# Performance work log

Hardware: AMD Instinct MI355X
Metric: run time of the kernel (lower is better)

## Reference

```python
import jax, jax.numpy as jnp
import numpy as np

B, T = 32, 64
INPUT_DIM, EMB, HA, HB, NUM_CLASS = 4894, 128, 128, 128, 1
D_IN = EMB + 1  # use_time=True appends scalar time feature


def gru_cell(x, h, Wih, Whh, bih, bhh):
    # torch nn.GRU cell semantics, gate order (r, z, n)
    gi = x @ Wih.T + bih
    gh = h @ Whh.T + bhh
    ir, iz, i_n = jnp.split(gi, 3, axis=-1)
    hr, hz, hn = jnp.split(gh, 3, axis=-1)
    r = jax.nn.sigmoid(ir + hr)
    z = jax.nn.sigmoid(iz + hz)
    n = jnp.tanh(i_n + r * hn)
    return (1.0 - z) * n + z * h


def setup_inputs():
    key = jax.random.key(0)
    ks = jax.random.split(key, 14)
    f32 = jnp.float32
    s = lambda k, sh, sc: (jax.random.normal(k, sh) * sc).astype(f32)
    return {
        "x": jax.random.uniform(ks[0], (B, T, INPUT_DIM), dtype=f32),
        "t": jax.random.uniform(ks[1], (B, T), dtype=f32),
        "lengths": jax.random.randint(ks[2], (B,), 1, T + 1),
        "W_emb": s(ks[3], (EMB, INPUT_DIM), 0.02),
        "Wih_a": s(ks[4], (3 * HA, D_IN), 0.05),
        "Whh_a": s(ks[5], (3 * HA, HA), 0.05),
        "bih_a": jnp.zeros((3 * HA,), f32),
        "bhh_a": jnp.zeros((3 * HA,), f32),
        "Wih_b": s(ks[6], (3 * HB, D_IN), 0.05),
        "Whh_b": s(ks[7], (3 * HB, HB), 0.05),
        "bih_b": jnp.zeros((3 * HB,), f32),
        "bhh_b": jnp.zeros((3 * HB,), f32),
        "w_alpha": s(ks[8], (1, HA), 0.1),
        "b_alpha": jnp.zeros((1,), f32),
        "W_beta": s(ks[9], (EMB, HB), 0.1),
        "b_beta": jnp.zeros((EMB,), f32),
        "W_out": s(ks[10], (NUM_CLASS, EMB), 0.1),
        "b_out": jnp.zeros((NUM_CLASS,), f32),
    }


def reference(x, t, lengths, W_emb, Wih_a, Whh_a, bih_a, bhh_a,
              Wih_b, Whh_b, bih_b, bhh_b, w_alpha, b_alpha,
              W_beta, b_beta, W_out, b_out):
    # embedding (dropout is identity in inference)
    emb = x @ W_emb.T                                   # [B,T,E]
    temb = jnp.concatenate([emb, t[..., None]], axis=-1)  # [B,T,E+1]

    # reversed-prefix tensor: R[b,i,k] = temb[b, i-k] for k<=i else 0
    i_idx = jnp.arange(T)[:, None]
    k_idx = jnp.arange(T)[None, :]
    src = i_idx - k_idx                                  # [T,T]
    valid = (src >= 0)
    src_c = jnp.clip(src, 0)
    vmask = valid[None, :, :, None].astype(emb.dtype)
    R = jnp.take(temb, src_c, axis=1) * vmask            # [B,T,T,D_IN]
    E_rev = jnp.take(emb, src_c, axis=1) * vmask         # [B,T,T,E]

    # run alpha/beta GRUs along the prefix axis k (causal, so zero padding
    # at k>i never affects the k<=i outputs that we keep)
    R_k = jnp.moveaxis(R, 2, 0)                          # [Tk,B,T,D_IN]
    h0a = jnp.zeros((B, T, HA), emb.dtype)
    h0b = jnp.zeros((B, T, HB), emb.dtype)

    def step(carry, xk):
        ha, hb = carry
        ha = gru_cell(xk, ha, Wih_a, Whh_a, bih_a, bhh_a)
        hb = gru_cell(xk, hb, Wih_b, Whh_b, bih_b, bhh_b)
        return (ha, hb), (ha, hb)

    _, (Ha, Hb) = jax.lax.scan(step, (h0a, h0b), R_k)
    Ha = jnp.moveaxis(Ha, 0, 2)                          # [B,T,Tk,HA]
    Hb = jnp.moveaxis(Hb, 0, 2)                          # [B,T,Tk,HB]

    # attention over the i+1 prefix positions
    scores = (Ha @ w_alpha.T + b_alpha)[..., 0]          # [B,T,Tk]
    scores = jnp.where(valid[None], scores, jnp.float32(-1e9))
    alpha = jax.nn.softmax(scores, axis=-1)
    beta = jnp.tanh(Hb @ W_beta.T + b_beta)              # [B,T,Tk,E]

    c = jnp.einsum('btk,btke,btke->bte', alpha, beta, E_rev)
    row_valid = (jnp.arange(T)[None, :] < lengths[:, None]).astype(c.dtype)
    c = c * row_valid[..., None]                         # zero where i >= lengths[b]

    logits = c @ W_out.T + b_out                         # [B,T,1]
    return logits[..., 0]
```

## Files before the change

### kernel.cpp

```cpp
#include <hip/hip_runtime.h>
#include <hip/hip_bf16.h>

#define DEVI __device__ __forceinline__

typedef __attribute__((ext_vector_type(8))) short short8;
typedef __attribute__((ext_vector_type(8))) unsigned short ushort8;
typedef __attribute__((ext_vector_type(4))) unsigned short ushort4v;
typedef __attribute__((ext_vector_type(2))) unsigned int u32x2;
typedef __attribute__((ext_vector_type(4))) float f32x4;

static constexpr int TT = 64, KIN = 4894, KINP = 4896, E = 128;
static constexpr float L2E = 1.4426950408889634f;

DEVI unsigned short f2bf(float f) {
    union { float f; unsigned u; } v; v.f = f;
    unsigned r = v.u + 0x7fffu + ((v.u >> 16) & 1u);
    return (unsigned short)(r >> 16);
}
DEVI float sigm2(float x) { return __builtin_amdgcn_rcpf(1.f + __builtin_amdgcn_exp2f(-x)); }
DEVI float tanh2(float x) { return 1.f - 2.f * __builtin_amdgcn_rcpf(__builtin_amdgcn_exp2f(x + x) + 1.f); }

DEVI void bar_lds() {
    asm volatile("s_waitcnt lgkmcnt(0)" ::: "memory");
    __builtin_amdgcn_s_barrier();
}

DEVI short8 cvt8(const float* __restrict__ p, float s) {
    float2 v0 = *(const float2*)p, v1 = *(const float2*)(p + 2);
    float2 v2 = *(const float2*)(p + 4), v3 = *(const float2*)(p + 6);
    short8 r;
    r[0] = (short)f2bf(v0.x * s); r[1] = (short)f2bf(v0.y * s);
    r[2] = (short)f2bf(v1.x * s); r[3] = (short)f2bf(v1.y * s);
    r[4] = (short)f2bf(v2.x * s); r[5] = (short)f2bf(v2.y * s);
    r[6] = (short)f2bf(v3.x * s); r[7] = (short)f2bf(v3.y * s);
    return r;
}

__global__ void prep_kernel(const float* __restrict__ Wemb,
                            const float* __restrict__ Wih_a, const float* __restrict__ Wih_b,
                            const float* __restrict__ Whh_a, const float* __restrict__ Whh_b,
                            const float* __restrict__ Wbeta,
                            unsigned short* __restrict__ wembbf, unsigned short* __restrict__ wihbf,
                            unsigned short* __restrict__ whhbf, unsigned short* __restrict__ wbetabf) {
    int job = blockIdx.x * blockDim.x + threadIdx.x;
    const int JWE = 128 * 612, JWIH = 768 * 16, JWHH = 768 * 16, JWB = 128 * 16;
    if (job < JWE) {
        int row = job / 612, c8 = (job % 612) * 8;
        ushort8 v;
        #pragma unroll
        for (int jj = 0; jj < 8; ++jj) { int c = c8 + jj; v[jj] = (c < KIN) ? f2bf(Wemb[(long)row * KIN + c]) : (unsigned short)0; }
        *(ushort8*)(wembbf + (long)row * KINP + c8) = v;
        return;
    }
    job -= JWE;
    if (job < JWIH) {
        int g = job / 16, c8 = (job % 16) * 8;
        const float* src = (g < 384) ? (Wih_a + (long)g * 129) : (Wih_b + (long)(g - 384) * 129);
        ushort8 v;
        #pragma unroll
        for (int jj = 0; jj < 8; ++jj) v[jj] = f2bf(src[c8 + jj] * L2E);
        *(ushort8*)(wihbf + (long)g * 128 + c8) = v;
        return;
    }
    job -= JWIH;
    if (job < JWHH) {
        int g = job / 16, c8 = (job % 16) * 8;
        const float* src = (g < 384) ? (Whh_a + (long)g * 128) : (Whh_b + (long)(g - 384) * 128);
        ushort8 v;
        #pragma unroll
        for (int jj = 0; jj < 8; ++jj) v[jj] = f2bf(src[c8 + jj] * L2E);
        *(ushort8*)(whhbf + (long)g * 128 + c8) = v;
        return;
    }
    job -= JWHH;
    if (job < JWB) {
        int e = job / 16, c8 = (job % 16) * 8;
        ushort8 v;
        #pragma unroll
        for (int jj = 0; jj < 8; ++jj) v[jj] = f2bf(Wbeta[(long)e * 128 + c8 + jj] * L2E);
        *(ushort8*)(wbetabf + (long)e * 128 + c8) = v;
    }
}

__global__ __launch_bounds__(256) void emb_gemm(const float* __restrict__ x,
                                                const unsigned short* __restrict__ wembbf,
                                                float* __restrict__ pout) {
    const int ks = blockIdx.x & 3, m0 = (blockIdx.x >> 2) * 16;
    const int w = threadIdx.x >> 6, l = threadIdx.x & 63, lr = l & 15, lo = l >> 4;
    const int n0 = (2 * w) * 16 + lr, n1 = (2 * w + 1) * 16 + lr;
    const float* xrow = x + (long)(m0 + lr) * KIN;
    const int k0 = ks * 1216;
    f32x4 acc0 = {0, 0, 0, 0}, acc1 = {0, 0, 0, 0};
    #pragma unroll 2
    for (int kt = 0; kt < 38; ++kt) {
        int k = k0 + kt * 32 + lo * 8;
        short8 a = cvt8(xrow + k, 1.f);
        short8 b0 = *(const short8*)(wembbf + (long)n0 * KINP + k);
        short8 b1 = *(const short8*)(wembbf + (long)n1 * KINP + k);
        acc0 = __builtin_amdgcn_mfma_f32_16x16x32_bf16(a, b0, acc0, 0, 0, 0);
        acc1 = __builtin_amdgcn_mfma_f32_16x16x32_bf16(a, b1, acc1, 0, 0, 0);
    }
    if (ks == 3) {
        int k = 4864 + lo * 8;
        short8 a;
        #pragma unroll
        for (int jj = 0; jj < 8; ++jj) { int c = k + jj; a[jj] = (c < KIN) ? (short)f2bf(xrow[c]) : (short)0; }
        short8 b0 = *(const short8*)(wembbf + (long)n0 * KINP + k);
        short8 b1 = *(const short8*)(wembbf + (long)n1 * KINP + k);
        acc0 = __builtin_amdgcn_mfma_f32_16x16x32_bf16(a, b0, acc0, 0, 0, 0);
        acc1 = __builtin_amdgcn_mfma_f32_16x16x32_bf16(a, b1, acc1, 0, 0, 0);
    }
    float* pbase = pout + (long)ks * 2048 * E;
    #pragma unroll
    for (int r = 0; r < 4; ++r) {
        int m = m0 + lo * 4 + r;
        pbase[(long)m * E + n0] = acc0[r];
        pbase[(long)m * E + n1] = acc1[r];
    }
}

__global__ __launch_bounds__(256) void emb_reduce(const float* __restrict__ pout,
                                                  float* __restrict__ emb, unsigned short* __restrict__ embbf) {
    const long idx = (long)blockIdx.x * 256 + threadIdx.x;
    const long base = idx * 4;
    f32x4 s = *(const f32x4*)(pout + base);
    #pragma unroll
    for (int ks = 1; ks < 4; ++ks) {
        f32x4 v = *(const f32x4*)(pout + (long)ks * 2048 * E + base);
        s[0] += v[0]; s[1] += v[1]; s[2] += v[2]; s[3] += v[3];
    }
    *(f32x4*)(emb + base) = s;
    ushort4v h;
    #pragma unroll
    for (int jj = 0; jj < 4; ++jj) h[jj] = f2bf(s[jj]);
    *(ushort4v*)(embbf + base) = h;
}

__global__ __launch_bounds__(256) void gi_gemm(const unsigned short* __restrict__ embbf,
                                               const unsigned short* __restrict__ wihbf,
                                               const float* __restrict__ Wih_a, const float* __restrict__ Wih_b,
                                               const float* __restrict__ t,
                                               const float* __restrict__ bih_a, const float* __restrict__ bih_b,
                                               const float* __restrict__ bhh_a, const float* __restrict__ bhh_b,
                                               float* __restrict__ Gi3) {
    const int m0 = blockIdx.x * 16;
    const int w = threadIdx.x >> 6, l = threadIdx.x & 63, lr = l & 15, lo = l >> 4;
    f32x4 acc[12];
    #pragma unroll
    for (int nl = 0; nl < 12; ++nl) acc[nl] = (f32x4){0, 0, 0, 0};
    #pragma unroll
    for (int kt = 0; kt < 4; ++kt) {
        int k = kt * 32 + lo * 8;
        short8 a0 = *(const short8*)(embbf + (long)(m0 + lr) * E + k);
        #pragma unroll
        for (int nl = 0; nl < 12; ++nl) {
            int n = (w * 12 + nl) * 16 + lr;
            short8 bf = *(const short8*)(wihbf + (long)n * 128 + k);
            acc[nl] = __builtin_amdgcn_mfma_f32_16x16x32_bf16(a0, bf, acc[nl], 0, 0, 0);
        }
    }
    #pragma unroll
    for (int nl = 0; nl < 12; ++nl) {
        int n = (w * 12 + nl) * 16 + lr;
        int gru = (n >= 384) ? 1 : 0;
        int nn = n - gru * 384;
        int gt = nn >> 7, u = nn & 127;
        float bias = (gru ? bih_b[nn] : bih_a[nn]);
        if (gt < 2) bias += (gru ? bhh_b[nn] : bhh_a[nn]);
        float cw = (n < 384) ? Wih_a[(long)n * 129 + 128] : Wih_b[(long)(n - 384) * 129 + 128];
        #pragma unroll
        for (int r = 0; r < 4; ++r) {
            int tok = m0 + lo * 4 + r;
            Gi3[((long)(tok * 2 + gru) * 128 + u) * 4 + gt] = acc[nl][r] + (bias + t[tok] * cw) * L2E;
        }
    }
}

__global__ __launch_bounds__(512) __attribute__((amdgpu_waves_per_eu(2, 2)))
void retain_rec(const unsigned short* __restrict__ whhbf, const unsigned short* __restrict__ wbetabf,
                const float* __restrict__ Gi3, const float* __restrict__ emb,
                const float* __restrict__ bhh_a, const float* __restrict__ bhh_b,
                const float* __restrict__ w_alpha, const float* __restrict__ b_alpha,
                const float* __restrict__ b_beta, const float* __restrict__ Wout,
                float* __restrict__ p_g, float* __restrict__ d_g) {
    const int tid = threadIdx.x;
    const int w = tid >> 6, l = tid & 63, lr = l & 15, lo = l >> 4;
    const int i = blockIdx.x >> 2, q = (blockIdx.x >> 1) & 1, g = blockIdx.x & 1;
    const int u0 = w * 16 + lo * 4;

    __shared__ __align__(16) unsigned short Hbf[2][16][128];
    __shared__ __align__(16) unsigned short Mld[2][16][128];
    __shared__ float pd_s[16][66];

    for (int idx = tid; idx < 2 * 16 * 128; idx += 512) (&Hbf[0][0][0])[idx] = 0;

    short8 Wf[3][4];
    #pragma unroll
    for (int gt = 0; gt < 3; ++gt)
        #pragma unroll
        for (int kt = 0; kt < 4; ++kt)
            Wf[gt][kt] = *(const short8*)(whhbf + (long)(g * 384 + gt * 128 + w * 16 + lr) * 128 + kt * 32 + lo * 8);
    short8 Xf[4];
    #pragma unroll
    for (int kt = 0; kt < 4; ++kt)
        Xf[kt] = g ? *(const short8*)(wbetabf + (long)(w * 16 + lr) * 128 + kt * 32 + lo * 8)
                   : cvt8(w_alpha + kt * 32 + lo * 8, L2E);
    short8 ones;
    #pragma unroll
    for (int jj = 0; jj < 8; ++jj) ones[jj] = (short)0x3F80;

    const float* bhhG = g ? bhh_b : bhh_a;
    f32x4 bhn4 = *(const f32x4*)(bhhG + 256 + u0);
    #pragma unroll
    for (int r = 0; r < 4; ++r) bhn4[r] *= L2E;
    f32x4 bb4 = {0, 0, 0, 0}, wo4 = {0, 0, 0, 0};
    if (g) {
        bb4 = *(const f32x4*)(b_beta + u0);
        #pragma unroll
        for (int r = 0; r < 4; ++r) bb4[r] *= L2E;
        wo4 = *(const f32x4*)(Wout + u0);
    }
    const float balL = b_alpha[0] * L2E;

    float h_old[4] = {0, 0, 0, 0};

    const int tok0 = (q * 16 + lr) * 64 + i;
    const f32x4* gp = (const f32x4*)Gi3 + ((long)(tok0 * 2 + g) * 128 + u0);
    const float* ep = emb + (long)tok0 * E + u0;
    f32x4 giv[4];
    #pragma unroll
    for (int r = 0; r < 4; ++r) giv[r] = gp[r];
    f32x4 ev = {0, 0, 0, 0};

    __syncthreads();

    const int iend = i + 1 + g;
    for (int n = 0; n <= iend; ++n) {
        const int rb = n & 1, wb = rb ^ 1;
        const bool do_gate = (n <= i);
        const bool do_post = (n >= 1) && (n <= i + 1);
        const bool ld_gi = (n < i);
        const bool ld_ev = g && (n <= i);

        f32x4 givn[4], evn;
        if (ld_gi) {
            gp -= 256;
            #pragma unroll
            for (int r = 0; r < 4; ++r) givn[r] = gp[r];
        }
        if (ld_ev) { evn = *(const f32x4*)ep; ep -= E; }

        if (g && w == 0 && n >= 2) {
            f32x4 dacc = {0, 0, 0, 0};
            #pragma unroll
            for (int kt = 0; kt < 4; ++kt) {
                int sw = (kt * 32 + lo * 8) ^ ((lr & 7) * 8);
                short8 bm = *(const short8*)(&Mld[wb][lr][sw]);
                dacc = __builtin_amdgcn_mfma_f32_16x16x32_bf16(ones, bm, dacc, 0, 0, 0);
            }
            if (lo == 0) pd_s[lr][n - 2] = dacc[0];
        }

        short8 Af[4];
        if (do_gate || do_post) {
            #pragma unroll
            for (int kt = 0; kt < 4; ++kt) {
                int sw = (kt * 32 + lo * 8) ^ ((lr & 7) * 8);
                Af[kt] = *(const short8*)(&Hbf[rb][lr][sw]);
            }
        }

        f32x4 gh0 = {0, 0, 0, 0}, gh1 = {0, 0, 0, 0}, gh2 = bhn4;
        if (do_gate) {
            #pragma unroll
            for (int kt = 0; kt < 4; ++kt) {
                gh0 = __builtin_amdgcn_mfma_f32_16x16x32_bf16(Wf[0][kt], Af[kt], gh0, 0, 0, 0);
                gh1 = __builtin_amdgcn_mfma_f32_16x16x32_bf16(Wf[1][kt], Af[kt], gh1, 0, 0, 0);
                gh2 = __builtin_amdgcn_mfma_f32_16x16x32_bf16(Wf[2][kt], Af[kt], gh2, 0, 0, 0);
            }
        }

        if (do_post) {
            f32x4 xacc = {0, 0, 0, 0};
            #pragma unroll
            for (int kt = 0; kt < 4; ++kt)
                xacc = __builtin_amdgcn_mfma_f32_16x16x32_bf16(Xf[kt], Af[kt], xacc, 0, 0, 0);
            if (!g) {
                if (w == 0 && lo == 0) pd_s[lr][n - 1] = __builtin_amdgcn_exp2f(xacc[0] + balL);
            } else {
                float m0v = tanh2(xacc[0] + bb4[0]) * ev[0] * wo4[0];
                float m1v = tanh2(xacc[1] + bb4[1]) * ev[1] * wo4[1];
                float m2v = tanh2(xacc[2] + bb4[2]) * ev[2] * wo4[2];
                float m3v = tanh2(xacc[3] + bb4[3]) * ev[3] * wo4[3];
                unsigned mp0, mp1;
                asm("v_cvt_pk_bf16_f32 %0, %1, %2" : "=v"(mp0) : "v"(m0v), "v"(m1v));
                asm("v_cvt_pk_bf16_f32 %0, %1, %2" : "=v"(mp1) : "v"(m2v), "v"(m3v));
                *(u32x2*)(&Mld[rb][lr][u0 ^ ((lr & 7) * 8)]) = (u32x2){mp0, mp1};
            }
        }

        if (do_gate) {
            float hn[4];
            #pragma unroll
            for (int r = 0; r < 4; ++r) {
                f32x4 gv = giv[r];
                float rr = sigm2(gv[0] + gh0[r]);
                float zz = sigm2(gv[1] + gh1[r]);
                float nv = tanh2(gv[2] + rr * gh2[r]);
                float h = nv + zz * (h_old[r] - nv);
                h_old[r] = h;
                hn[r] = h;
            }
            unsigned p0, p1;
            asm("v_cvt_pk_bf16_f32 %0, %1, %2" : "=v"(p0) : "v"(hn[0]), "v"(hn[1]));
            asm("v_cvt_pk_bf16_f32 %0, %1, %2" : "=v"(p1) : "v"(hn[2]), "v"(hn[3]));
            *(u32x2*)(&Hbf[wb][lr][u0 ^ ((lr & 7) * 8)]) = (u32x2){p0, p1};
        }

        if (ld_gi) {
            #pragma unroll
            for (int r = 0; r < 4; ++r) giv[r] = givn[r];
        }
        if (ld_ev) ev = evn;

        bar_lds();
    }

    float* dst = g ? d_g : p_g;
    for (int idx = tid; idx < 16 * 64; idx += 512) {
        int c = idx >> 6, kk = idx & 63;
        if (kk <= i) {
            long row = (long)(q * 16 + c) * 64 + i;
            dst[row * 64 + kk] = pd_s[c][kk];
        }
    }
}

__global__ __launch_bounds__(512) void reduce_out(const float* __restrict__ p_g, const float* __restrict__ d_g,
                                                  const int* __restrict__ lengths, const float* __restrict__ b_out,
                                                  float* __restrict__ out) {
    const int w = threadIdx.x >> 6, l = threadIdx.x & 63;
    const int row = blockIdx.x * 8 + w;
    const int b = row >> 6, i = row & 63;
    float p = (l <= i) ? p_g[(long)row * 64 + l] : 0.f;
    float d = (l <= i) ? d_g[(long)row * 64 + l] : 0.f;
    float pd = p * d;
    #pragma unroll
    for (int off = 1; off < 64; off <<= 1) {
        p += __shfl_xor(p, off);
        pd += __shfl_xor(pd, off);
    }
    if (l == 0) {
        float val = (i < lengths[b]) ? pd / p + b_out[0] : b_out[0];
        out[row] = val;
    }
}

extern "C" void kernel_launch(void* const* d_in, const int* in_sizes, int n_in,
                              void* d_out, int out_size, void* d_ws, size_t ws_size,
                              hipStream_t stream) {
    (void)in_sizes; (void)n_in; (void)out_size; (void)ws_size;
    const float* x       = (const float*)d_in[0];
    const float* t       = (const float*)d_in[1];
    const int*   len     = (const int*)d_in[2];
    const float* Wemb    = (const float*)d_in[3];
    const float* Wih_a   = (const float*)d_in[4];
    const float* Whh_a   = (const float*)d_in[5];
    const float* bih_a   = (const float*)d_in[6];
    const float* bhh_a   = (const float*)d_in[7];
    const float* Wih_b   = (const float*)d_in[8];
    const float* Whh_b   = (const float*)d_in[9];
    const float* bih_b   = (const float*)d_in[10];
    const float* bhh_b   = (const float*)d_in[11];
    const float* w_alpha = (const float*)d_in[12];
    const float* b_alpha = (const float*)d_in[13];
    const float* W_beta  = (const float*)d_in[14];
    const float* b_beta  = (const float*)d_in[15];
    const float* W_out   = (const float*)d_in[16];
    const float* b_out   = (const float*)d_in[17];

    char* ws = (char*)d_ws;
    float*          emb     = (float*)(ws + 0);
    unsigned short* embbf   = (unsigned short*)(ws + 1048576);
    float*          Gi3     = (float*)(ws + 1572864);
    unsigned short* wembbf  = (unsigned short*)(ws + 9961472);
    unsigned short* wihbf   = (unsigned short*)(ws + 11214848);
    unsigned short* whhbf   = (unsigned short*)(ws + 11411456);
    unsigned short* wbetabf = (unsigned short*)(ws + 11608064);
    float*          p_g     = (float*)(ws + 11640832);
    float*          d_g     = (float*)(ws + 12165120);
    float*          pout    = (float*)(ws + 12689408);

    const int jobs = 128 * 612 + 768 * 16 + 768 * 16 + 128 * 16;
    prep_kernel<<<(jobs + 255) / 256, 256, 0, stream>>>(Wemb, Wih_a, Wih_b, Whh_a, Whh_b, W_beta,
                                                        wembbf, wihbf, whhbf, wbetabf);
    emb_gemm<<<512, 256, 0, stream>>>(x, wembbf, pout);
    emb_reduce<<<256, 256, 0, stream>>>(pout, emb, embbf);
    gi_gemm<<<128, 256, 0, stream>>>(embbf, wihbf, Wih_a, Wih_b, t, bih_a, bih_b, bhh_a, bhh_b, Gi3);
    retain_rec<<<256, 512, 0, stream>>>(whhbf, wbetabf, Gi3, emb, bhh_a, bhh_b,
                                        w_alpha, b_alpha, b_beta, W_out, p_g, d_g);
    reduce_out<<<256, 512, 0, stream>>>(p_g, d_g, len, b_out, (float*)d_out);
}
```

Before: 164.5 us.

## Stage GRU input gates and embeddings into LDS via async global_load_lds double buffering

```diff
diff --git a/kernel.cpp b/kernel.cpp
--- a/kernel.cpp
+++ b/kernel.cpp
@@ -20,9 +20,10 @@
 DEVI float sigm2(float x) { return __builtin_amdgcn_rcpf(1.f + __builtin_amdgcn_exp2f(-x)); }
 DEVI float tanh2(float x) { return 1.f - 2.f * __builtin_amdgcn_rcpf(__builtin_amdgcn_exp2f(x + x) + 1.f); }
 
-DEVI void bar_lds() {
-    asm volatile("s_waitcnt lgkmcnt(0)" ::: "memory");
-    __builtin_amdgcn_s_barrier();
+DEVI void gload16(const float* g, float* l) {
+    __builtin_amdgcn_global_load_lds(
+        (const __attribute__((address_space(1))) void*)g,
+        (__attribute__((address_space(3))) void*)l, 16, 0, 0);
 }
 
 DEVI short8 cvt8(const float* __restrict__ p, float s) {
@@ -120,7 +121,7 @@
 }
 
 __global__ __launch_bounds__(256) void emb_reduce(const float* __restrict__ pout,
-                                                  float* __restrict__ emb, unsigned short* __restrict__ embbf) {
+                                                  float* __restrict__ emb_swz, unsigned short* __restrict__ embbf) {
     const long idx = (long)blockIdx.x * 256 + threadIdx.x;
     const long base = idx * 4;
     f32x4 s = *(const f32x4*)(pout + base);
@@ -129,7 +130,10 @@
         f32x4 v = *(const f32x4*)(pout + (long)ks * 2048 * E + base);
         s[0] += v[0]; s[1] += v[1]; s[2] += v[2]; s[3] += v[3];
     }
-    *(f32x4*)(emb + base) = s;
+    const long tok = base >> 7;
+    const int e0 = (int)(base & 127);
+    const int cc = (int)((tok >> 6) & 15);
+    *(f32x4*)(emb_swz + (tok << 7) + (e0 ^ ((cc & 7) << 2))) = s;
     ushort4v h;
     #pragma unroll
     for (int jj = 0; jj < 4; ++jj) h[jj] = f2bf(s[jj]);
@@ -171,14 +175,16 @@
         #pragma unroll
         for (int r = 0; r < 4; ++r) {
             int tok = m0 + lo * 4 + r;
-            Gi3[((long)(tok * 2 + gru) * 128 + u) * 4 + gt] = acc[nl][r] + (bias + t[tok] * cw) * L2E;
-        }
-    }
-}
-
-__global__ __launch_bounds__(512) __attribute__((amdgpu_waves_per_eu(2, 2)))
+            int cc = (tok >> 6) & 15;
+            Gi3[(((long)tok * 2 + gru) * 3 + gt) * 128 + (u ^ ((cc & 7) << 2))] =
+                acc[nl][r] + (bias + t[tok] * cw) * L2E;
+        }
+    }
+}
+
+__global__ __launch_bounds__(512, 1)
 void retain_rec(const unsigned short* __restrict__ whhbf, const unsigned short* __restrict__ wbetabf,
-                const float* __restrict__ Gi3, const float* __restrict__ emb,
+                const float* __restrict__ Gi3, const float* __restrict__ emb_swz,
                 const float* __restrict__ bhh_a, const float* __restrict__ bhh_b,
                 const float* __restrict__ w_alpha, const float* __restrict__ b_alpha,
                 const float* __restrict__ b_beta, const float* __restrict__ Wout,
@@ -187,7 +193,11 @@
     const int w = tid >> 6, l = tid & 63, lr = l & 15, lo = l >> 4;
     const int i = blockIdx.x >> 2, q = (blockIdx.x >> 1) & 1, g = blockIdx.x & 1;
     const int u0 = w * 16 + lo * 4;
-
+    const int sw2 = (lr & 7) << 2;
+    const int cS = tid >> 5, chk = tid & 31;
+
+    __shared__ __align__(16) float Gst[2][3][16][128];
+    __shared__ __align__(16) float Est[2][16][128];
     __shared__ __align__(16) unsigned short Hbf[2][16][128];
     __shared__ __align__(16) unsigned short Mld[2][16][128];
     __shared__ float pd_s[16][66];
@@ -224,31 +234,31 @@
 
     float h_old[4] = {0, 0, 0, 0};
 
-    const int tok0 = (q * 16 + lr) * 64 + i;
-    const f32x4* gp = (const f32x4*)Gi3 + ((long)(tok0 * 2 + g) * 128 + u0);
-    const float* ep = emb + (long)tok0 * E + u0;
-    f32x4 giv[4];
-    #pragma unroll
-    for (int r = 0; r < 4; ++r) giv[r] = gp[r];
-    f32x4 ev = {0, 0, 0, 0};
-
-    __syncthreads();
+    const long chainBase = (long)((q * 16 + cS) * 64);
+    auto STAGE = [&](int b, int jg, int je) {
+        const float* gb = Gi3 + ((chainBase + jg) * 2 + g) * 384 + chk * 4;
+        float* lds0 = (float*)&Gst[b][0][0][0] + (w << 8);
+        gload16(gb, lds0);
+        gload16(gb + 128, (float*)&Gst[b][1][0][0] + (w << 8));
+        gload16(gb + 256, (float*)&Gst[b][2][0][0] + (w << 8));
+        if (g) gload16(emb_swz + ((chainBase + je) << 7) + chk * 4, (float*)&Est[b][0][0] + (w << 8));
+    };
+
+    STAGE(0, i, (i + 1 > 63) ? 63 : i + 1);
 
     const int iend = i + 1 + g;
     for (int n = 0; n <= iend; ++n) {
-        const int rb = n & 1, wb = rb ^ 1;
+        __syncthreads();
+
+        {
+            int jg = i - n - 1; if (jg < 0) jg = 0;
+            int je = i - n;     if (je < 0) je = 0;
+            STAGE((n + 1) & 1, jg, je);
+        }
+
+        const int rb = n & 1, wb = rb ^ 1, bufc = n & 1;
         const bool do_gate = (n <= i);
         const bool do_post = (n >= 1) && (n <= i + 1);
-        const bool ld_gi = (n < i);
-        const bool ld_ev = g && (n <= i);
-
-        f32x4 givn[4], evn;
-        if (ld_gi) {
-            gp -= 256;
-            #pragma unroll
-            for (int r = 0; r < 4; ++r) givn[r] = gp[r];
-        }
-        if (ld_ev) { evn = *(const f32x4*)ep; ep -= E; }
 
         if (g && w == 0 && n >= 2) {
             f32x4 dacc = {0, 0, 0, 0};
@@ -272,26 +282,37 @@
 
         f32x4 gh0 = {0, 0, 0, 0}, gh1 = {0, 0, 0, 0}, gh2 = bhn4;
         if (do_gate) {
-            #pragma unroll
-            for (int kt = 0; kt < 4; ++kt) {
+            f32x4 a0 = {0, 0, 0, 0}, a1 = {0, 0, 0, 0}, a2 = {0, 0, 0, 0};
+            #pragma unroll
+            for (int kt = 0; kt < 2; ++kt) {
                 gh0 = __builtin_amdgcn_mfma_f32_16x16x32_bf16(Wf[0][kt], Af[kt], gh0, 0, 0, 0);
                 gh1 = __builtin_amdgcn_mfma_f32_16x16x32_bf16(Wf[1][kt], Af[kt], gh1, 0, 0, 0);
                 gh2 = __builtin_amdgcn_mfma_f32_16x16x32_bf16(Wf[2][kt], Af[kt], gh2, 0, 0, 0);
-            }
+                a0 = __builtin_amdgcn_mfma_f32_16x16x32_bf16(Wf[0][kt + 2], Af[kt + 2], a0, 0, 0, 0);
+                a1 = __builtin_amdgcn_mfma_f32_16x16x32_bf16(Wf[1][kt + 2], Af[kt + 2], a1, 0, 0, 0);
+                a2 = __builtin_amdgcn_mfma_f32_16x16x32_bf16(Wf[2][kt + 2], Af[kt + 2], a2, 0, 0, 0);
+            }
+            #pragma unroll
+            for (int r = 0; r < 4; ++r) { gh0[r] += a0[r]; gh1[r] += a1[r]; gh2[r] += a2[r]; }
         }
 
         if (do_post) {
-            f32x4 xacc = {0, 0, 0, 0};
-            #pragma unroll
-            for (int kt = 0; kt < 4; ++kt)
+            f32x4 xacc = {0, 0, 0, 0}, xb = {0, 0, 0, 0};
+            #pragma unroll
+            for (int kt = 0; kt < 2; ++kt) {
                 xacc = __builtin_amdgcn_mfma_f32_16x16x32_bf16(Xf[kt], Af[kt], xacc, 0, 0, 0);
+                xb   = __builtin_amdgcn_mfma_f32_16x16x32_bf16(Xf[kt + 2], Af[kt + 2], xb, 0, 0, 0);
+            }
+            #pragma unroll
+            for (int r = 0; r < 4; ++r) xacc[r] += xb[r];
             if (!g) {
                 if (w == 0 && lo == 0) pd_s[lr][n - 1] = __builtin_amdgcn_exp2f(xacc[0] + balL);
             } else {
-                float m0v = tanh2(xacc[0] + bb4[0]) * ev[0] * wo4[0];
-                float m1v = tanh2(xacc[1] + bb4[1]) * ev[1] * wo4[1];
-                float m2v = tanh2(xacc[2] + bb4[2]) * ev[2] * wo4[2];
-                float m3v = tanh2(xacc[3] + bb4[3]) * ev[3] * wo4[3];
+                f32x4 ev4 = *(const f32x4*)(&Est[bufc][lr][u0 ^ sw2]);
+                float m0v = tanh2(xacc[0] + bb4[0]) * ev4[0] * wo4[0];
+                float m1v = tanh2(xacc[1] + bb4[1]) * ev4[1] * wo4[1];
+                float m2v = tanh2(xacc[2] + bb4[2]) * ev4[2] * wo4[2];
+                float m3v = tanh2(xacc[3] + bb4[3]) * ev4[3] * wo4[3];
                 unsigned mp0, mp1;
                 asm("v_cvt_pk_bf16_f32 %0, %1, %2" : "=v"(mp0) : "v"(m0v), "v"(m1v));
                 asm("v_cvt_pk_bf16_f32 %0, %1, %2" : "=v"(mp1) : "v"(m2v), "v"(m3v));
@@ -300,13 +321,15 @@
         }
 
         if (do_gate) {
+            f32x4 gr = *(const f32x4*)(&Gst[bufc][0][lr][u0 ^ sw2]);
+            f32x4 gz = *(const f32x4*)(&Gst[bufc][1][lr][u0 ^ sw2]);
+            f32x4 gn = *(const f32x4*)(&Gst[bufc][2][lr][u0 ^ sw2]);
             float hn[4];
             #pragma unroll
             for (int r = 0; r < 4; ++r) {
-                f32x4 gv = giv[r];
-                float rr = sigm2(gv[0] + gh0[r]);
-                float zz = sigm2(gv[1] + gh1[r]);
-                float nv = tanh2(gv[2] + rr * gh2[r]);
+                float rr = sigm2(gr[r] + gh0[r]);
+                float zz = sigm2(gz[r] + gh1[r]);
+                float nv = tanh2(gn[r] + rr * gh2[r]);
                 float h = nv + zz * (h_old[r] - nv);
                 h_old[r] = h;
                 hn[r] = h;
@@ -316,15 +339,9 @@
             asm("v_cvt_pk_bf16_f32 %0, %1, %2" : "=v"(p1) : "v"(hn[2]), "v"(hn[3]));
             *(u32x2*)(&Hbf[wb][lr][u0 ^ ((lr & 7) * 8)]) = (u32x2){p0, p1};
         }
-
-        if (ld_gi) {
-            #pragma unroll
-            for (int r = 0; r < 4; ++r) giv[r] = givn[r];
-        }
-        if (ld_ev) ev = evn;
-
-        bar_lds();
-    }
+    }
+
+    __syncthreads();
 
     float* dst = g ? d_g : p_g;
     for (int idx = tid; idx < 16 * 64; idx += 512) {
@@ -380,24 +397,24 @@
     const float* b_out   = (const float*)d_in[17];
 
     char* ws = (char*)d_ws;
-    float*          emb     = (float*)(ws + 0);
+    float*          emb_swz = (float*)(ws + 0);
     unsigned short* embbf   = (unsigned short*)(ws + 1048576);
     float*          Gi3     = (float*)(ws + 1572864);
-    unsigned short* wembbf  = (unsigned short*)(ws + 9961472);
-    unsigned short* wihbf   = (unsigned short*)(ws + 11214848);
-    unsigned short* whhbf   = (unsigned short*)(ws + 11411456);
-    unsigned short* wbetabf = (unsigned short*)(ws + 11608064);
-    float*          p_g     = (float*)(ws + 11640832);
-    float*          d_g     = (float*)(ws + 12165120);
-    float*          pout    = (float*)(ws + 12689408);
+    unsigned short* wembbf  = (unsigned short*)(ws + 7864320);
+    unsigned short* wihbf   = (unsigned short*)(ws + 9117696);
+    unsigned short* whhbf   = (unsigned short*)(ws + 9314304);
+    unsigned short* wbetabf = (unsigned short*)(ws + 9510912);
+    float*          p_g     = (float*)(ws + 9543680);
+    float*          d_g     = (float*)(ws + 10067968);
+    float*          pout    = (float*)(ws + 10592256);
 
     const int jobs = 128 * 612 + 768 * 16 + 768 * 16 + 128 * 16;
     prep_kernel<<<(jobs + 255) / 256, 256, 0, stream>>>(Wemb, Wih_a, Wih_b, Whh_a, Whh_b, W_beta,
                                                         wembbf, wihbf, whhbf, wbetabf);
     emb_gemm<<<512, 256, 0, stream>>>(x, wembbf, pout);
-    emb_reduce<<<256, 256, 0, stream>>>(pout, emb, embbf);
+    emb_reduce<<<256, 256, 0, stream>>>(pout, emb_swz, embbf);
     gi_gemm<<<128, 256, 0, stream>>>(embbf, wihbf, Wih_a, Wih_b, t, bih_a, bih_b, bhh_a, bhh_b, Gi3);
-    retain_rec<<<256, 512, 0, stream>>>(whhbf, wbetabf, Gi3, emb, bhh_a, bhh_b,
+    retain_rec<<<256, 512, 0, stream>>>(whhbf, wbetabf, Gi3, emb_swz, bhh_a, bhh_b,
                                         w_alpha, b_alpha, b_beta, W_out, p_g, d_g);
     reduce_out<<<256, 512, 0, stream>>>(p_g, d_g, len, b_out, (float*)d_out);
 }
```

Result: faster. 134.6 us (-18.2%).
